# Performance work log

Hardware: AMD Instinct MI355X
Metric: run time of the kernel (lower is better)

The kernel has to match this reference:

```python
import jax, jax.numpy as jnp
import numpy as np

B, S, IN_DIM, D, H, L, C = 8, 1024, 256, 1024, 16, 6, 10
DK = D // H
EPS = 1e-5


def setup_inputs() -> dict:
    key = jax.random.key(0)
    ks = iter(jax.random.split(key, 64))
    n = lambda shape, s=0.02: jax.random.normal(next(ks), shape, dtype=jnp.float32) * s
    inp = {
        'x': jax.random.normal(next(ks), (B, S, IN_DIM), dtype=jnp.float32),
        'emb_w': n((IN_DIM, D)), 'emb_b': jnp.zeros((D,), jnp.float32),
        'Wq': n((L, D, D)), 'bq': jnp.zeros((L, D), jnp.float32),
        'Wk': n((L, D, D)), 'bk': jnp.zeros((L, D), jnp.float32),
        'Wv': n((L, D, D)), 'bv': jnp.zeros((L, D), jnp.float32),
        'Wo': n((L, D, D)), 'bo': jnp.zeros((L, D), jnp.float32),
        'W1': n((L, D, 4 * D)), 'b1': jnp.zeros((L, 4 * D), jnp.float32),
        'W2': n((L, 4 * D, D)), 'b2': jnp.zeros((L, D), jnp.float32),
        'ln1_s': jnp.ones((L, D), jnp.float32), 'ln1_b': jnp.zeros((L, D), jnp.float32),
        'ln2_s': jnp.ones((L, D), jnp.float32), 'ln2_b': jnp.zeros((L, D), jnp.float32),
        'fc_w': n((D, C)), 'fc_b': jnp.zeros((C,), jnp.float32),
    }
    return inp


def _pos_encoding_rows(n_rows):
    # Faithful to the torch module: pe is [max_len,1,D]; pe[:x.size(0)] picks the
    # first `batch` positions and broadcasts over the sequence dim.
    pos = jnp.arange(n_rows, dtype=jnp.float32)[:, None]
    div = jnp.exp(jnp.arange(0, D, 2, dtype=jnp.float32) * (-np.log(10000.0) / D))
    pe = jnp.zeros((n_rows, D), jnp.float32)
    pe = pe.at[:, 0::2].set(jnp.sin(pos * div)).at[:, 1::2].set(jnp.cos(pos * div))
    return pe


def _layer_norm(x, scale, bias):
    mu = jnp.mean(x, axis=-1, keepdims=True)
    var = jnp.mean(jnp.square(x - mu), axis=-1, keepdims=True)
    return (x - mu) * jax.lax.rsqrt(var + EPS) * scale + bias


def reference(x, emb_w, emb_b, Wq, bq, Wk, bk, Wv, bv, Wo, bo,
              W1, b1, W2, b2, ln1_s, ln1_b, ln2_s, ln2_b, fc_w, fc_b):
    h = x @ emb_w + emb_b                              # [B,S,D]
    h = h + _pos_encoding_rows(B)[:, None, :]          # broadcast pe[:B] over seq
    scale = 1.0 / np.sqrt(DK)
    for i in range(L):
        def heads(y, W, b):
            return (y @ W + b).reshape(B, S, H, DK).transpose(0, 2, 1, 3)  # bhsd
        q = heads(h, Wq[i], bq[i])
        k = heads(h, Wk[i], bk[i])
        v = heads(h, Wv[i], bv[i])
        scores = jnp.einsum('bhqd,bhkd->bhqk', q, k) * scale
        p = jax.nn.softmax(scores, axis=-1)
        o = jnp.einsum('bhqk,bhkd->bhqd', p, v)
        o = o.transpose(0, 2, 1, 3).reshape(B, S, D)
        attn_out = o @ Wo[i] + bo[i]
        h = _layer_norm(h + attn_out, ln1_s[i], ln1_b[i])
        ff = jax.nn.relu(h @ W1[i] + b1[i]) @ W2[i] + b2[i]
        h = _layer_norm(h + ff, ln2_s[i], ln2_b[i])
    pooled = jnp.mean(h, axis=1)                       # [B,D]
    return pooled @ fc_w + fc_b                        # [B,C]
```

## Files before the change

kernel.cpp:

```cpp
#include <hip/hip_runtime.h>
#include <stdint.h>

#define B_   8
#define S_   1024
#define IND  256
#define D_   1024
#define H_   16
#define DKH  64
#define L_   6
#define FF   4096
#define NTOK (B_*S_)

typedef __bf16 bf16;
typedef __attribute__((ext_vector_type(4))) float  f32x4;
typedef __attribute__((ext_vector_type(8))) __bf16 bf16x8;
typedef __attribute__((ext_vector_type(4))) __bf16 bf16x4;
typedef __attribute__((ext_vector_type(2))) __bf16 bf16x2;

#define AS1 __attribute__((address_space(1)))
#define AS3 __attribute__((address_space(3)))

__device__ __forceinline__ void gload16(const void* g, void* l) {
  __builtin_amdgcn_global_load_lds((AS1 void*)(const_cast<void*>(g)), (AS3 void*)l, 16, 0, 0);
}

__global__ __launch_bounds__(256)
void k_trans(const float* __restrict__ in, bf16* __restrict__ out,
             int K, int N, long inStride, long outStride) {
  __shared__ float t[32][33];
  const float* inp = in + (long)blockIdx.z * inStride;
  bf16* outp = out + (long)blockIdx.z * outStride;
  const int n0 = blockIdx.x * 32, k0 = blockIdx.y * 32;
  const int tx = threadIdx.x & 31, ty = threadIdx.x >> 5;
  #pragma unroll
  for (int j = 0; j < 32; j += 8)
    t[ty + j][tx] = inp[(long)(k0 + ty + j) * N + n0 + tx];
  __syncthreads();
  #pragma unroll
  for (int j = 0; j < 32; j += 8)
    outp[(long)(n0 + ty + j) * K + k0 + tx] = (bf16)t[tx][ty + j];
}

__global__ __launch_bounds__(256)
void k_f2b(const float* __restrict__ in, bf16* __restrict__ out) {
  const long i = ((long)blockIdx.x * 256 + threadIdx.x) * 4;
  f32x4 v = *(const f32x4*)(in + i);
  bf16x4 o;
  #pragma unroll
  for (int j = 0; j < 4; ++j) o[j] = (bf16)v[j];
  *(bf16x4*)(out + i) = o;
}

__global__ __launch_bounds__(256)
void k_pe(float* __restrict__ pe) {
  const int i = blockIdx.x * 256 + threadIdx.x;
  const int b = i >> 10, d = i & 1023;
  const float k2 = (float)(d & ~1);
  const float dv = __expf(k2 * (-9.210340371976184f / (float)D_));
  const float a = (float)b * dv;
  pe[i] = (d & 1) ? cosf(a) : sinf(a);
}

__global__ __launch_bounds__(256)
void k_packb(const float* __restrict__ bq, const float* __restrict__ bk,
             const float* __restrict__ bv, float* __restrict__ out) {
  const int i = blockIdx.x * 256 + threadIdx.x;
  const int l = i / 3072, j = i % 3072;
  const float* src = (j < 1024) ? bq : ((j < 2048) ? bk : bv);
  out[i] = src[l * 1024 + (j & 1023)];
}

template<int EPI>
__global__ __launch_bounds__(256)
void k_gemm(const bf16* __restrict__ A, const bf16* __restrict__ Bt,
            const float* __restrict__ bias,
            void* __restrict__ out0, void* __restrict__ out1,
            const float* __restrict__ pe,
            int M, int N, int K) {
  __shared__ __align__(16) bf16 sA[128 * 32];
  __shared__ __align__(16) bf16 sB[128 * 32];
  const int tid = threadIdx.x;
  const int lane = tid & 63, wv = tid >> 6;
  const int bx = blockIdx.x, by = blockIdx.y;
  const int wm = wv >> 1, wn = wv & 1;
  const int lg = lane >> 4, lc = lane & 15;
  const long arow0 = (long)by * 128;
  const long brow0 = (long)bx * 128;
  const int c0 = (wv * 2 + 0) * 64 + lane;
  const int c1 = (wv * 2 + 1) * 64 + lane;
  const int r0 = c0 >> 2, s0 = c0 & 3;
  const int r1 = c1 >> 2, s1 = c1 & 3;
  bf16* ldsA0 = sA + (wv * 2 + 0) * 512;
  bf16* ldsA1 = sA + (wv * 2 + 1) * 512;
  bf16* ldsB0 = sB + (wv * 2 + 0) * 512;
  bf16* ldsB1 = sB + (wv * 2 + 1) * 512;
  const bf16* Ab = A + arow0 * K;
  const bf16* Bb = Bt + brow0 * K;
  f32x4 acc[4][4] = {};
  const int kT = K >> 5;
  for (int kt = 0; kt < kT; ++kt) {
    const int k0 = kt << 5;
    gload16(Ab + (long)r0 * K + k0 + s0 * 8, ldsA0);
    gload16(Ab + (long)r1 * K + k0 + s1 * 8, ldsA1);
    gload16(Bb + (long)r0 * K + k0 + s0 * 8, ldsB0);
    gload16(Bb + (long)r1 * K + k0 + s1 * 8, ldsB1);
    __syncthreads();
    bf16x8 af[4], bfr[4];
    #pragma unroll
    for (int mr = 0; mr < 4; ++mr)
      af[mr] = *(const bf16x8*)(sA + (wm * 64 + mr * 16 + lc) * 32 + lg * 8);
    #pragma unroll
    for (int nc = 0; nc < 4; ++nc)
      bfr[nc] = *(const bf16x8*)(sB + (wn * 64 + nc * 16 + lc) * 32 + lg * 8);
    #pragma unroll
    for (int mr = 0; mr < 4; ++mr)
      #pragma unroll
      for (int nc = 0; nc < 4; ++nc)
        acc[mr][nc] = __builtin_amdgcn_mfma_f32_16x16x32_bf16(af[mr], bfr[nc], acc[mr][nc], 0, 0, 0);
    __syncthreads();
  }
  #pragma unroll
  for (int mr = 0; mr < 4; ++mr) {
    const int row0 = by * 128 + wm * 64 + mr * 16 + lg * 4;
    #pragma unroll
    for (int nc = 0; nc < 4; ++nc) {
      const int col = bx * 128 + wn * 64 + nc * 16 + lc;
      const float bvv = bias[col];
      #pragma unroll
      for (int r = 0; r < 4; ++r) {
        float v = acc[mr][nc][r] + bvv;
        const long rr = row0 + r;
        if constexpr (EPI == 0) {
          ((bf16*)out0)[rr * N + col] = (bf16)v;
        } else {
          const long bb = rr >> 10;
          v += pe[bb * D_ + col];
          ((float*)out0)[rr * N + col] = v;
          ((bf16*)out1)[rr * N + col] = (bf16)v;
        }
      }
    }
  }
}

template<int EPI, int SPLIT>
__global__ __launch_bounds__(512, 2)
void k_gemm256(const bf16* __restrict__ A, const bf16* __restrict__ Bt,
               const float* __restrict__ bias,
               void* __restrict__ out0, void* __restrict__ out1,
               bf16* __restrict__ pout0, bf16* __restrict__ pout1,
               int M, int N, int K) {
  __shared__ __align__(16) bf16 lds[65536];
  const int tid = threadIdx.x;
  const int lane = tid & 63, wv = tid >> 6;
  const int wm = wv >> 2, wn = wv & 3;
  const int lg = lane >> 4, lc = lane & 15;
  const int gx = gridDim.x;
  const int nwg = gx * gridDim.y;
  int bid = blockIdx.x + blockIdx.y * gx;
  const int cpx = nwg >> 3;
  bid = (bid & 7) * cpx + (bid >> 3);
  const int bxs = bid % gx, bys = bid / gx;
  const int tileRow = bys * 256, tileCol = bxs * 256;
  const int kPart = SPLIT ? (K >> 1) : K;
  const long kOff = SPLIT ? (long)blockIdx.z * kPart : 0;
  const bf16* Abase = A + (long)tileRow * K + kOff;
  const bf16* Bbase = Bt + (long)tileCol * K + kOff;
  const long laneOff = (long)lc * K + lg * 8;
  f32x4 acc[8][4] = {};
  const int NT = kPart >> 6;
  const int NI = NT >> 1;

  auto stA = [&](int t, int h, int bb) {
    const int rg = h * 16 + wv * 2;
    const int mb = rg >> 1;
    const bf16* s = Abase + (long)(mb * 16) * K + t * 64 + laneOff;
    bf16* d = lds + bb * 32768 + rg * 512;
    gload16(s, d);
    gload16(s + 32, d + 512);
  };
  auto stB = [&](int t, int h, int bb) {
    const int rg = h * 16 + wv * 2;
    const int mb = rg >> 1;
    const bf16* s = Bbase + (long)(mb * 16) * K + t * 64 + laneOff;
    bf16* d = lds + bb * 32768 + 16384 + rg * 512;
    gload16(s, d);
    gload16(s + 32, d + 512);
  };

  bf16x8 aF[8];
  bf16x8 bF0[4], bF1[4];

#define LDA(BB, MH) do { _Pragma("unroll") for (int m = 0; m < 4; ++m) \
    _Pragma("unroll") for (int kk = 0; kk < 2; ++kk) \
      aF[m*2+kk] = *(const bf16x8*)(lds + (BB)*32768 + ((wm*8 + (MH)*4 + m)*2 + kk)*512 + lane*8); \
  } while(0)
#define LDB(BB, NH, DST) do { _Pragma("unroll") for (int n = 0; n < 2; ++n) \
    _Pragma("unroll") for (int kk = 0; kk < 2; ++kk) \
      DST[n*2+kk] = *(const bf16x8*)(lds + (BB)*32768 + 16384 + ((wn*4 + (NH)*2 + n)*2 + kk)*512 + lane*8); \
  } while(0)
#define MMA(MH, NH, BSRC) do { \
    __builtin_amdgcn_s_setprio(1); \
    _Pragma("unroll") for (int m = 0; m < 4; ++m) \
      _Pragma("unroll") for (int n = 0; n < 2; ++n) { \
        acc[(MH)*4+m][(NH)*2+n] = __builtin_amdgcn_mfma_f32_16x16x32_bf16(aF[m*2+0], BSRC[n*2+0], acc[(MH)*4+m][(NH)*2+n], 0, 0, 0); \
        acc[(MH)*4+m][(NH)*2+n] = __builtin_amdgcn_mfma_f32_16x16x32_bf16(aF[m*2+1], BSRC[n*2+1], acc[(MH)*4+m][(NH)*2+n], 0, 0, 0); \
      } \
    __builtin_amdgcn_s_setprio(0); \
  } while(0)
#define VM8 asm volatile("s_waitcnt vmcnt(8)" ::: "memory")
#define VM0 asm volatile("s_waitcnt vmcnt(0)" ::: "memory")
#define BAR __builtin_amdgcn_s_barrier()

  stA(0, 0, 0); stB(0, 0, 0); stA(0, 1, 0); stB(0, 1, 0);
  stA(1, 0, 1); stB(1, 0, 1); stA(1, 1, 1); stB(1, 1, 1);

  for (int i = 0; i < NI - 1; ++i) {
    const int t2 = 2 * i + 2, t3 = 2 * i + 3;
    VM8; BAR; LDA(0, 0); LDB(0, 0, bF0);   MMA(0, 0, bF0);
         BAR; LDB(0, 1, bF1); stA(t2, 0, 0);              MMA(0, 1, bF1);
         BAR; LDA(0, 1);      stB(t2, 0, 0);              MMA(1, 0, bF0);
         BAR; stA(t2, 1, 0);  stB(t2, 1, 0);              MMA(1, 1, bF1);
    VM8; BAR; LDA(1, 0); LDB(1, 0, bF0);   MMA(0, 0, bF0);
         BAR; LDB(1, 1, bF1); stA(t3, 0, 1);              MMA(0, 1, bF1);
         BAR; LDA(1, 1);      stB(t3, 0, 1);              MMA(1, 0, bF0);
         BAR; stA(t3, 1, 1);  stB(t3, 1, 1);              MMA(1, 1, bF1);
  }
  {
    VM8; BAR; LDA(0, 0); LDB(0, 0, bF0); MMA(0, 0, bF0);
         BAR; LDB(0, 1, bF1);            MMA(0, 1, bF1);
         BAR; LDA(0, 1);                 MMA(1, 0, bF0);
         BAR;                            MMA(1, 1, bF1);
    VM0; BAR; LDA(1, 0); LDB(1, 0, bF0); MMA(0, 0, bF0);
         BAR; LDB(1, 1, bF1);            MMA(0, 1, bF1);
         BAR; LDA(1, 1);                 MMA(1, 0, bF0);
         BAR;                            MMA(1, 1, bF1);
  }
#undef LDA
#undef LDB
#undef MMA
#undef VM8
#undef VM0
#undef BAR

  #pragma unroll
  for (int mr = 0; mr < 8; ++mr) {
    const int row0 = tileRow + wm * 128 + mr * 16 + lg * 4;
    #pragma unroll
    for (int nr = 0; nr < 4; ++nr) {
      const int col = tileCol + wn * 64 + nr * 16 + lc;
      if constexpr (SPLIT) {
        bf16* po = blockIdx.z ? pout1 : pout0;
        #pragma unroll
        for (int r = 0; r < 4; ++r)
          po[(long)(row0 + r) * N + col] = (bf16)acc[mr][nr][r];
      } else if constexpr (EPI == 2) {
        const float bvv = bias[col];
        const int which = col >> 10;
        const int hh = (col & 1023) >> 6;
        const int dk = col & 63;
        const long bb = row0 >> 10;
        const int sr = row0 & 1023;
        if (which == 2) {
          bf16x4 pk;
          #pragma unroll
          for (int r = 0; r < 4; ++r) pk[r] = (bf16)(acc[mr][nr][r] + bvv);
          *(bf16x4*)((bf16*)out1 + ((bb * H_ + hh) * (long)DKH + dk) * S_ + sr) = pk;
        } else {
          #pragma unroll
          for (int r = 0; r < 4; ++r) {
            float v = acc[mr][nr][r] + bvv;
            if (which == 0) v *= 0.125f;
            ((bf16*)out0)[(long)which * NTOK * D_ + ((bb * H_ + hh) * (long)S_ + sr + r) * DKH + dk] = (bf16)v;
          }
        }
      } else {
        const float bvv = bias[col];
        #pragma unroll
        for (int r = 0; r < 4; ++r) {
          float v = acc[mr][nr][r] + bvv;
          const long rr = row0 + r;
          if constexpr (EPI == 1) v = fmaxf(v, 0.f);
          ((bf16*)out0)[rr * N + col] = (bf16)v;
        }
      }
    }
  }
}

__global__ __launch_bounds__(256)
void k_flash(const bf16* __restrict__ qg, const bf16* __restrict__ kgl,
             const bf16* __restrict__ vtg, bf16* __restrict__ og) {
  __shared__ __align__(16) bf16 sK[64 * 64];
  __shared__ __align__(16) bf16 sV[64 * 64];
  __shared__ __align__(16) bf16 sP[4 * 16 * 64];
  const int tid = threadIdx.x, lane = tid & 63, wv = tid >> 6;
  const int lg = lane >> 4, lc = lane & 15;
  int bid = blockIdx.x + blockIdx.y * 16;
  bid = (bid & 7) * 256 + (bid >> 3);
  const int qt = bid & 15, bh = bid >> 4;
  const long base = (long)bh * S_ * DKH;
  const bf16* qb = qg + base;
  const bf16* kb = kgl + base;
  const bf16* vb = vtg + base;
  const int qrow = qt * 64 + wv * 16 + lc;
  const bf16x8 qf0 = *(const bf16x8*)(qb + (long)qrow * DKH + lg * 8);
  const bf16x8 qf1 = *(const bf16x8*)(qb + (long)qrow * DKH + 32 + lg * 8);
  float mrun = -3e38f, lrun = 0.f;
  f32x4 oacc[4] = {};
  bf16* sPw = sP + wv * (16 * 64);
  const int swzP = (lc & 7) << 4;
  const int c0 = wv * 128 + lane, c1 = c0 + 64;
  const int r0 = c0 >> 3, sl0 = (c0 & 7) ^ (r0 & 7);
  const int r1 = c1 >> 3, sl1 = (c1 & 7) ^ (r1 & 7);
  bf16* dst0 = sK + c0 * 8 - lane * 8;
  bf16* dst1 = sK + c1 * 8 - lane * 8;
  bf16* dstV0 = sV + c0 * 8 - lane * 8;
  bf16* dstV1 = sV + c1 * 8 - lane * 8;
  for (int kt = 0; kt < S_ / 64; ++kt) {
    const int gk = kt * 64;
    gload16(kb + (long)(gk + r0) * DKH + sl0 * 8, dst0);
    gload16(kb + (long)(gk + r1) * DKH + sl1 * 8, dst1);
    gload16(vb + (long)r0 * S_ + gk + sl0 * 8, dstV0);
    gload16(vb + (long)r1 * S_ + gk + sl1 * 8, dstV1);
    __syncthreads();
    f32x4 sacc[4] = {};
    #pragma unroll
    for (int nc = 0; nc < 4; ++nc) {
      const int kr = nc * 16 + lc;
      bf16x8 k0 = *(const bf16x8*)((char*)sK + kr * 128 + (((0 + lg) ^ (kr & 7)) << 4));
      bf16x8 k1 = *(const bf16x8*)((char*)sK + kr * 128 + (((4 + lg) ^ (kr & 7)) << 4));
      sacc[nc] = __builtin_amdgcn_mfma_f32_16x16x32_bf16(k0, qf0, sacc[nc], 0, 0, 0);
      sacc[nc] = __builtin_amdgcn_mfma_f32_16x16x32_bf16(k1, qf1, sacc[nc], 0, 0, 0);
    }
    float pm = sacc[0][0];
    #pragma unroll
    for (int nc = 0; nc < 4; ++nc)
      #pragma unroll
      for (int r = 0; r < 4; ++r) pm = fmaxf(pm, sacc[nc][r]);
    pm = fmaxf(pm, __shfl_xor(pm, 16));
    pm = fmaxf(pm, __shfl_xor(pm, 32));
    const float mnew = fmaxf(mrun, pm);
    const float fac = __expf(mrun - mnew);
    float ps = 0.f;
    #pragma unroll
    for (int nc = 0; nc < 4; ++nc)
      #pragma unroll
      for (int r = 0; r < 4; ++r) {
        const float p = __expf(sacc[nc][r] - mnew);
        sacc[nc][r] = p;
        ps += p;
      }
    ps += __shfl_xor(ps, 16);
    ps += __shfl_xor(ps, 32);
    lrun = lrun * fac + ps;
    mrun = mnew;
    #pragma unroll
    for (int nc = 0; nc < 4; ++nc)
      #pragma unroll
      for (int rp = 0; rp < 2; ++rp) {
        bf16x2 t;
        t[0] = (bf16)sacc[nc][rp * 2 + 0];
        t[1] = (bf16)sacc[nc][rp * 2 + 1];
        *(bf16x2*)((char*)sPw + lc * 128 + ((nc * 32 + lg * 8 + rp * 4) ^ swzP)) = t;
      }
    asm volatile("s_waitcnt lgkmcnt(0)" ::: "memory");
    __builtin_amdgcn_sched_barrier(0);
    float fr[4];
    #pragma unroll
    for (int r = 0; r < 4; ++r) fr[r] = __shfl(fac, lg * 4 + r);
    #pragma unroll
    for (int nc = 0; nc < 4; ++nc)
      #pragma unroll
      for (int r = 0; r < 4; ++r) oacc[nc][r] *= fr[r];
    #pragma unroll
    for (int m = 0; m < 2; ++m) {
      const bf16x8 pf = *(const bf16x8*)((char*)sPw + lc * 128 + ((m * 64 + lg * 16) ^ swzP));
      #pragma unroll
      for (int nc = 0; nc < 4; ++nc) {
        const int vr = nc * 16 + lc;
        bf16x8 vf = *(const bf16x8*)((char*)sV + vr * 128 + (((m * 4 + lg) ^ (vr & 7)) << 4));
        oacc[nc] = __builtin_amdgcn_mfma_f32_16x16x32_bf16(pf, vf, oacc[nc], 0, 0, 0);
      }
    }
    __syncthreads();
  }
  const int b = bh >> 4, h = bh & 15;
  const float linv = 1.f / lrun;
  #pragma unroll
  for (int r = 0; r < 4; ++r) {
    const float inv = __shfl(linv, lg * 4 + r);
    const int s = qt * 64 + wv * 16 + lg * 4 + r;
    const long obase = (((long)b * S_ + s) * H_ + h) * DKH;
    #pragma unroll
    for (int nc = 0; nc < 4; ++nc)
      og[obase + nc * 16 + lc] = (bf16)(oacc[nc][r] * inv);
  }
}

template<int TWO>
__global__ __launch_bounds__(256)
void k_addln(const float* __restrict__ hin, const bf16* __restrict__ dlt,
             const bf16* __restrict__ p0, const bf16* __restrict__ p1,
             const float* __restrict__ gb,
             const float* __restrict__ sc, const float* __restrict__ bi,
             float* __restrict__ hout, bf16* __restrict__ hbout) {
  const int row = blockIdx.x, t = threadIdx.x;
  const long off = (long)row * D_ + t * 4;
  f32x4 hv = *(const f32x4*)(hin + off);
  f32x4 x;
  if constexpr (TWO) {
    bf16x4 a = *(const bf16x4*)(p0 + off);
    bf16x4 b = *(const bf16x4*)(p1 + off);
    f32x4 g = *(const f32x4*)(gb + t * 4);
    #pragma unroll
    for (int j = 0; j < 4; ++j) x[j] = hv[j] + (float)a[j] + (float)b[j] + g[j];
  } else {
    bf16x4 dv = *(const bf16x4*)(dlt + off);
    #pragma unroll
    for (int j = 0; j < 4; ++j) x[j] = hv[j] + (float)dv[j];
  }
  float s = 0.f, ss = 0.f;
  #pragma unroll
  for (int j = 0; j < 4; ++j) { s += x[j]; ss += x[j] * x[j]; }
  #pragma unroll
  for (int m = 1; m < 64; m <<= 1) { s += __shfl_xor(s, m); ss += __shfl_xor(ss, m); }
  __shared__ float red[8];
  const int w = t >> 6, ln = t & 63;
  if (ln == 0) { red[w] = s; red[4 + w] = ss; }
  __syncthreads();
  s = red[0] + red[1] + red[2] + red[3];
  ss = red[4] + red[5] + red[6] + red[7];
  const float mu = s * (1.f / D_);
  const float rstd = rsqrtf(ss * (1.f / D_) - mu * mu + 1e-5f);
  f32x4 scv = *(const f32x4*)(sc + t * 4);
  f32x4 biv = *(const f32x4*)(bi + t * 4);
  f32x4 y; bf16x4 yb;
  #pragma unroll
  for (int j = 0; j < 4; ++j) { y[j] = (x[j] - mu) * rstd * scv[j] + biv[j]; yb[j] = (bf16)y[j]; }
  *(f32x4*)(hout + off) = y;
  *(bf16x4*)(hbout + off) = yb;
}

__global__ __launch_bounds__(256)
void k_pool1(const float* __restrict__ h, float* __restrict__ part) {
  const int i = blockIdx.x * 256 + threadIdx.x;
  const int b = i >> 10, d = i & 1023;
  const int s0 = blockIdx.y * 128;
  float s = 0.f;
  for (int t = 0; t < 128; ++t) s += h[((long)b * S_ + s0 + t) * D_ + d];
  part[(long)blockIdx.y * NTOK + i] = s;
}

__global__ __launch_bounds__(256)
void k_pool2(const float* __restrict__ part, float* __restrict__ pooled) {
  const int i = blockIdx.x * 256 + threadIdx.x;
  float s = 0.f;
  #pragma unroll
  for (int j = 0; j < 8; ++j) s += part[(long)j * NTOK + i];
  pooled[i] = s * (1.f / S_);
}

__global__ __launch_bounds__(64)
void k_fc(const float* __restrict__ pooled, const float* __restrict__ fw,
          const float* __restrict__ fb, float* __restrict__ out) {
  const int b = blockIdx.x / 10, c = blockIdx.x % 10;
  const int lane = threadIdx.x;
  float s = 0.f;
  for (int d = lane; d < D_; d += 64) s += pooled[b * D_ + d] * fw[d * 10 + c];
  #pragma unroll
  for (int m = 1; m < 64; m <<= 1) s += __shfl_xor(s, m);
  if (lane == 0) out[b * 10 + c] = s + fb[c];
}

extern "C" void kernel_launch(void* const* d_in, const int* in_sizes, int n_in,
                              void* d_out, int out_size, void* d_ws, size_t ws_size,
                              hipStream_t stream) {
  const float* x     = (const float*)d_in[0];
  const float* emb_w = (const float*)d_in[1];
  const float* emb_b = (const float*)d_in[2];
  const float* Wq    = (const float*)d_in[3];
  const float* bq    = (const float*)d_in[4];
  const float* Wk    = (const float*)d_in[5];
  const float* bk    = (const float*)d_in[6];
  const float* Wv    = (const float*)d_in[7];
  const float* bv    = (const float*)d_in[8];
  const float* Wo    = (const float*)d_in[9];
  const float* bo    = (const float*)d_in[10];
  const float* W1    = (const float*)d_in[11];
  const float* b1    = (const float*)d_in[12];
  const float* W2    = (const float*)d_in[13];
  const float* b2    = (const float*)d_in[14];
  const float* ln1s  = (const float*)d_in[15];
  const float* ln1b  = (const float*)d_in[16];
  const float* ln2s  = (const float*)d_in[17];
  const float* ln2b  = (const float*)d_in[18];
  const float* fcw   = (const float*)d_in[19];
  const float* fcb   = (const float*)d_in[20];

  char* w = (char*)d_ws;
  size_t off = 0;
  auto alloc = [&](size_t bytes) -> char* {
    char* p = w + off;
    off += (bytes + 255) & ~(size_t)255;
    return p;
  };
  bf16*  x_bf  = (bf16*) alloc((size_t)NTOK * IND * 2);
  bf16*  embT  = (bf16*) alloc((size_t)D_ * IND * 2);
  bf16*  qkvT  = (bf16*) alloc((size_t)L_ * 3 * D_ * D_ * 2);
  bf16*  woT   = (bf16*) alloc((size_t)L_ * D_ * D_ * 2);
  bf16*  w1T   = (bf16*) alloc((size_t)L_ * FF * D_ * 2);
  bf16*  w2T   = (bf16*) alloc((size_t)L_ * D_ * FF * 2);
  float* qkvB  = (float*)alloc((size_t)L_ * 3 * D_ * 4);
  float* pe    = (float*)alloc((size_t)B_ * D_ * 4);
  float* h_f   = (float*)alloc((size_t)NTOK * D_ * 4);
  bf16*  h_b   = (bf16*) alloc((size_t)NTOK * D_ * 2);
  bf16*  delta = (bf16*) alloc((size_t)NTOK * D_ * 2);
  float* pooled= (float*)alloc((size_t)B_ * D_ * 4);
  float* part  = (float*)alloc((size_t)8 * NTOK * 4);
  bf16*  scratch = (bf16*)alloc((size_t)NTOK * FF * 2);
  bf16* qb  = scratch;
  bf16* kb  = scratch + (size_t)NTOK * D_;
  bf16* vTb = scratch + (size_t)2 * NTOK * D_;
  bf16* ob  = scratch + (size_t)3 * NTOK * D_;
  bf16* ffn1 = scratch;
  bf16* p0 = (bf16*)alloc((size_t)NTOK * D_ * 2);
  bf16* p1 = (bf16*)alloc((size_t)NTOK * D_ * 2);
  const bool canSplit = (off <= ws_size);
  (void)in_sizes; (void)n_in; (void)out_size;

  k_f2b<<<dim3(NTOK * IND / 1024), dim3(256), 0, stream>>>(x, x_bf);
  k_trans<<<dim3(D_ / 32, IND / 32, 1), dim3(256), 0, stream>>>(emb_w, embT, IND, D_, 0, 0);
  k_trans<<<dim3(32, 32, L_), dim3(256), 0, stream>>>(Wq, qkvT,               D_, D_, (long)D_ * D_, (long)3 * D_ * D_);
  k_trans<<<dim3(32, 32, L_), dim3(256), 0, stream>>>(Wk, qkvT + D_ * D_,     D_, D_, (long)D_ * D_, (long)3 * D_ * D_);
  k_trans<<<dim3(32, 32, L_), dim3(256), 0, stream>>>(Wv, qkvT + 2 * D_ * D_, D_, D_, (long)D_ * D_, (long)3 * D_ * D_);
  k_trans<<<dim3(32, 32, L_), dim3(256), 0, stream>>>(Wo, woT, D_, D_, (long)D_ * D_, (long)D_ * D_);
  k_trans<<<dim3(FF / 32, 32, L_), dim3(256), 0, stream>>>(W1, w1T, D_, FF, (long)D_ * FF, (long)FF * D_);
  k_trans<<<dim3(32, FF / 32, L_), dim3(256), 0, stream>>>(W2, w2T, FF, D_, (long)FF * D_, (long)D_ * FF);
  k_pe<<<dim3(B_ * D_ / 256), dim3(256), 0, stream>>>(pe);
  k_packb<<<dim3(L_ * 3 * D_ / 256), dim3(256), 0, stream>>>(bq, bk, bv, qkvB);

  k_gemm<3><<<dim3(D_ / 128, NTOK / 128), dim3(256), 0, stream>>>(
      x_bf, embT, emb_b, h_f, h_b, pe, NTOK, D_, IND);

  for (int l = 0; l < L_; ++l) {
    k_gemm256<2, 0><<<dim3(3 * D_ / 256, NTOK / 256), dim3(512), 0, stream>>>(
        h_b, qkvT + (size_t)l * 3 * D_ * D_, qkvB + l * 3 * D_,
        qb, vTb, nullptr, nullptr, NTOK, 3 * D_, D_);
    k_flash<<<dim3(S_ / 64, B_ * H_), dim3(256), 0, stream>>>(qb, kb, vTb, ob);
    if (canSplit) {
      k_gemm256<0, 1><<<dim3(D_ / 256, NTOK / 256, 2), dim3(512), 0, stream>>>(
          ob, woT + (size_t)l * D_ * D_, nullptr,
          nullptr, nullptr, p0, p1, NTOK, D_, D_);
      k_addln<1><<<dim3(NTOK), dim3(256), 0, stream>>>(
          h_f, nullptr, p0, p1, bo + l * D_, ln1s + l * D_, ln1b + l * D_, h_f, h_b);
    } else {
      k_gemm256<0, 0><<<dim3(D_ / 256, NTOK / 256), dim3(512), 0, stream>>>(
          ob, woT + (size_t)l * D_ * D_, bo + l * D_,
          delta, nullptr, nullptr, nullptr, NTOK, D_, D_);
      k_addln<0><<<dim3(NTOK), dim3(256), 0, stream>>>(
          h_f, delta, nullptr, nullptr, nullptr, ln1s + l * D_, ln1b + l * D_, h_f, h_b);
    }
    k_gemm256<1, 0><<<dim3(FF / 256, NTOK / 256), dim3(512), 0, stream>>>(
        h_b, w1T + (size_t)l * FF * D_, b1 + l * FF,
        ffn1, nullptr, nullptr, nullptr, NTOK, FF, D_);
    if (canSplit) {
      k_gemm256<0, 1><<<dim3(D_ / 256, NTOK / 256, 2), dim3(512), 0, stream>>>(
          ffn1, w2T + (size_t)l * D_ * FF, nullptr,
          nullptr, nullptr, p0, p1, NTOK, D_, FF);
      k_addln<1><<<dim3(NTOK), dim3(256), 0, stream>>>(
          h_f, nullptr, p0, p1, b2 + l * D_, ln2s + l * D_, ln2b + l * D_, h_f, h_b);
    } else {
      k_gemm256<0, 0><<<dim3(D_ / 256, NTOK / 256), dim3(512), 0, stream>>>(
          ffn1, w2T + (size_t)l * D_ * FF, b2 + l * D_,
          delta, nullptr, nullptr, nullptr, NTOK, D_, FF);
      k_addln<0><<<dim3(NTOK), dim3(256), 0, stream>>>(
          h_f, delta, nullptr, nullptr, nullptr, ln2s + l * D_, ln2b + l * D_, h_f, h_b);
    }
  }

  k_pool1<<<dim3(NTOK / 256, 8), dim3(256), 0, stream>>>(h_f, part);
  k_pool2<<<dim3(NTOK / 256), dim3(256), 0, stream>>>(part, pooled);
  k_fc<<<dim3(B_ * 10), dim3(64), 0, stream>>>(pooled, fcw, fcb, (float*)d_out);
}
```

Before: 2.287 ms.

## Drop fp32 residual stream and add 128x256-tile QKV GEMM kernel

The fp32 copy of the hidden state is removed, so the residual add, layer norm and pooling now read and write only the bf16 activation buffer. This cuts memory traffic in the add+layernorm kernels and the embedding epilogue. It also adds a dedicated QKV projection GEMM with 128x256 tiles and a head-split epilogue, which doubles the number of workgroups for better CU occupancy. The price is lower residual precision, since bf16 rounding now accumulates across layers.

```diff
diff --git a/kernel.cpp b/kernel.cpp
--- a/kernel.cpp
+++ b/kernel.cpp
@@ -135,7 +135,6 @@
         } else {
           const long bb = rr >> 10;
           v += pe[bb * D_ + col];
-          ((float*)out0)[rr * N + col] = v;
           ((bf16*)out1)[rr * N + col] = (bf16)v;
         }
       }
@@ -254,26 +253,6 @@
         #pragma unroll
         for (int r = 0; r < 4; ++r)
           po[(long)(row0 + r) * N + col] = (bf16)acc[mr][nr][r];
-      } else if constexpr (EPI == 2) {
-        const float bvv = bias[col];
-        const int which = col >> 10;
-        const int hh = (col & 1023) >> 6;
-        const int dk = col & 63;
-        const long bb = row0 >> 10;
-        const int sr = row0 & 1023;
-        if (which == 2) {
-          bf16x4 pk;
-          #pragma unroll
-          for (int r = 0; r < 4; ++r) pk[r] = (bf16)(acc[mr][nr][r] + bvv);
-          *(bf16x4*)((bf16*)out1 + ((bb * H_ + hh) * (long)DKH + dk) * S_ + sr) = pk;
-        } else {
-          #pragma unroll
-          for (int r = 0; r < 4; ++r) {
-            float v = acc[mr][nr][r] + bvv;
-            if (which == 0) v *= 0.125f;
-            ((bf16*)out0)[(long)which * NTOK * D_ + ((bb * H_ + hh) * (long)S_ + sr + r) * DKH + dk] = (bf16)v;
-          }
-        }
       } else {
         const float bvv = bias[col];
         #pragma unroll
@@ -282,6 +261,127 @@
           const long rr = row0 + r;
           if constexpr (EPI == 1) v = fmaxf(v, 0.f);
           ((bf16*)out0)[rr * N + col] = (bf16)v;
+        }
+      }
+    }
+  }
+}
+
+__global__ __launch_bounds__(512, 2)
+void k_gemmQ(const bf16* __restrict__ A, const bf16* __restrict__ Bt,
+             const float* __restrict__ bias,
+             bf16* __restrict__ out0, bf16* __restrict__ out1,
+             int M, int N, int K) {
+  __shared__ __align__(16) bf16 lds[49152];
+  const int tid = threadIdx.x;
+  const int lane = tid & 63, wv = tid >> 6;
+  const int wm = wv >> 2, wn = wv & 3;
+  const int lg = lane >> 4, lc = lane & 15;
+  const int gx = gridDim.x;
+  const int nwg = gx * gridDim.y;
+  int bid = blockIdx.x + blockIdx.y * gx;
+  const int cpx = nwg >> 3;
+  bid = (bid & 7) * cpx + (bid >> 3);
+  const int bxs = bid % gx, bys = bid / gx;
+  const int tileRow = bys * 128, tileCol = bxs * 256;
+  const bf16* Abase = A + (long)tileRow * K;
+  const bf16* Bbase = Bt + (long)tileCol * K;
+  const long laneOff = (long)lc * K + lg * 8;
+  f32x4 acc[4][4] = {};
+  const int NT = K >> 6;
+  const int NI = NT >> 1;
+
+  auto stA = [&](int t, int bb) {
+    const bf16* s = Abase + (long)(wv * 16) * K + t * 64 + laneOff;
+    bf16* d = lds + bb * 24576 + (wv * 2) * 512;
+    gload16(s, d);
+    gload16(s + 32, d + 512);
+  };
+  auto stB = [&](int t, int h, int bb) {
+    const bf16* s = Bbase + (long)((wv * 2 + h) * 16) * K + t * 64 + laneOff;
+    bf16* d = lds + bb * 24576 + 8192 + (wv * 4 + h * 2) * 512;
+    gload16(s, d);
+    gload16(s + 32, d + 512);
+  };
+
+  bf16x8 aF[4];
+  bf16x8 bF0[4], bF1[4];
+
+#define LDA(BB, MH) do { _Pragma("unroll") for (int m = 0; m < 2; ++m) \
+    _Pragma("unroll") for (int kk = 0; kk < 2; ++kk) \
+      aF[m*2+kk] = *(const bf16x8*)(lds + (BB)*24576 + ((wm*4 + (MH)*2 + m)*2 + kk)*512 + lane*8); \
+  } while(0)
+#define LDB(BB, NH, DST) do { _Pragma("unroll") for (int n = 0; n < 2; ++n) \
+    _Pragma("unroll") for (int kk = 0; kk < 2; ++kk) \
+      DST[n*2+kk] = *(const bf16x8*)(lds + (BB)*24576 + 8192 + ((wn*4 + (NH)*2 + n)*2 + kk)*512 + lane*8); \
+  } while(0)
+#define MMA(MH, NH, BSRC) do { \
+    __builtin_amdgcn_s_setprio(1); \
+    _Pragma("unroll") for (int m = 0; m < 2; ++m) \
+      _Pragma("unroll") for (int n = 0; n < 2; ++n) { \
+        acc[(MH)*2+m][(NH)*2+n] = __builtin_amdgcn_mfma_f32_16x16x32_bf16(aF[m*2+0], BSRC[n*2+0], acc[(MH)*2+m][(NH)*2+n], 0, 0, 0); \
+        acc[(MH)*2+m][(NH)*2+n] = __builtin_amdgcn_mfma_f32_16x16x32_bf16(aF[m*2+1], BSRC[n*2+1], acc[(MH)*2+m][(NH)*2+n], 0, 0, 0); \
+      } \
+    __builtin_amdgcn_s_setprio(0); \
+  } while(0)
+#define VM6 asm volatile("s_waitcnt vmcnt(6)" ::: "memory")
+#define VM0 asm volatile("s_waitcnt vmcnt(0)" ::: "memory")
+#define BAR __builtin_amdgcn_s_barrier()
+
+  stA(0, 0); stB(0, 0, 0); stB(0, 1, 0);
+  stA(1, 1); stB(1, 0, 1); stB(1, 1, 1);
+
+  for (int i = 0; i < NI - 1; ++i) {
+    const int t2 = 2 * i + 2, t3 = 2 * i + 3;
+    VM6; BAR; LDA(0, 0); LDB(0, 0, bF0);   MMA(0, 0, bF0);
+         BAR; LDB(0, 1, bF1); stA(t2, 0);              MMA(0, 1, bF1);
+         BAR; LDA(0, 1);      stB(t2, 0, 0);           MMA(1, 0, bF0);
+         BAR;                 stB(t2, 1, 0);           MMA(1, 1, bF1);
+    VM6; BAR; LDA(1, 0); LDB(1, 0, bF0);   MMA(0, 0, bF0);
+         BAR; LDB(1, 1, bF1); stA(t3, 1);              MMA(0, 1, bF1);
+         BAR; LDA(1, 1);      stB(t3, 0, 1);           MMA(1, 0, bF0);
+         BAR;                 stB(t3, 1, 1);           MMA(1, 1, bF1);
+  }
+  {
+    VM6; BAR; LDA(0, 0); LDB(0, 0, bF0); MMA(0, 0, bF0);
+         BAR; LDB(0, 1, bF1);            MMA(0, 1, bF1);
+         BAR; LDA(0, 1);                 MMA(1, 0, bF0);
+         BAR;                            MMA(1, 1, bF1);
+    VM0; BAR; LDA(1, 0); LDB(1, 0, bF0); MMA(0, 0, bF0);
+         BAR; LDB(1, 1, bF1);            MMA(0, 1, bF1);
+         BAR; LDA(1, 1);                 MMA(1, 0, bF0);
+         BAR;                            MMA(1, 1, bF1);
+  }
+#undef LDA
+#undef LDB
+#undef MMA
+#undef VM6
+#undef VM0
+#undef BAR
+
+  #pragma unroll
+  for (int mr = 0; mr < 4; ++mr) {
+    const int row0 = tileRow + wm * 64 + mr * 16 + lg * 4;
+    #pragma unroll
+    for (int nr = 0; nr < 4; ++nr) {
+      const int col = tileCol + wn * 64 + nr * 16 + lc;
+      const float bvv = bias[col];
+      const int which = col >> 10;
+      const int hh = (col & 1023) >> 6;
+      const int dk = col & 63;
+      const long bb = row0 >> 10;
+      const int sr = row0 & 1023;
+      if (which == 2) {
+        bf16x4 pk;
+        #pragma unroll
+        for (int r = 0; r < 4; ++r) pk[r] = (bf16)(acc[mr][nr][r] + bvv);
+        *(bf16x4*)(out1 + ((bb * H_ + hh) * (long)DKH + dk) * S_ + sr) = pk;
+      } else {
+        #pragma unroll
+        for (int r = 0; r < 4; ++r) {
+          float v = acc[mr][nr][r] + bvv;
+          if (which == 0) v *= 0.125f;
+          out0[(long)which * NTOK * D_ + ((bb * H_ + hh) * (long)S_ + sr + r) * DKH + dk] = (bf16)v;
         }
       }
     }
@@ -400,25 +500,25 @@
 
 template<int TWO>
 __global__ __launch_bounds__(256)
-void k_addln(const float* __restrict__ hin, const bf16* __restrict__ dlt,
+void k_addln(const bf16* __restrict__ hin, const bf16* __restrict__ dlt,
              const bf16* __restrict__ p0, const bf16* __restrict__ p1,
              const float* __restrict__ gb,
              const float* __restrict__ sc, const float* __restrict__ bi,
-             float* __restrict__ hout, bf16* __restrict__ hbout) {
+             bf16* __restrict__ hbout) {
   const int row = blockIdx.x, t = threadIdx.x;
   const long off = (long)row * D_ + t * 4;
-  f32x4 hv = *(const f32x4*)(hin + off);
+  bf16x4 hv = *(const bf16x4*)(hin + off);
   f32x4 x;
   if constexpr (TWO) {
     bf16x4 a = *(const bf16x4*)(p0 + off);
     bf16x4 b = *(const bf16x4*)(p1 + off);
     f32x4 g = *(const f32x4*)(gb + t * 4);
     #pragma unroll
-    for (int j = 0; j < 4; ++j) x[j] = hv[j] + (float)a[j] + (float)b[j] + g[j];
+    for (int j = 0; j < 4; ++j) x[j] = (float)hv[j] + (float)a[j] + (float)b[j] + g[j];
   } else {
     bf16x4 dv = *(const bf16x4*)(dlt + off);
     #pragma unroll
-    for (int j = 0; j < 4; ++j) x[j] = hv[j] + (float)dv[j];
+    for (int j = 0; j < 4; ++j) x[j] = (float)hv[j] + (float)dv[j];
   }
   float s = 0.f, ss = 0.f;
   #pragma unroll
@@ -435,20 +535,19 @@
   const float rstd = rsqrtf(ss * (1.f / D_) - mu * mu + 1e-5f);
   f32x4 scv = *(const f32x4*)(sc + t * 4);
   f32x4 biv = *(const f32x4*)(bi + t * 4);
-  f32x4 y; bf16x4 yb;
-  #pragma unroll
-  for (int j = 0; j < 4; ++j) { y[j] = (x[j] - mu) * rstd * scv[j] + biv[j]; yb[j] = (bf16)y[j]; }
-  *(f32x4*)(hout + off) = y;
+  bf16x4 yb;
+  #pragma unroll
+  for (int j = 0; j < 4; ++j) yb[j] = (bf16)((x[j] - mu) * rstd * scv[j] + biv[j]);
   *(bf16x4*)(hbout + off) = yb;
 }
 
 __global__ __launch_bounds__(256)
-void k_pool1(const float* __restrict__ h, float* __restrict__ part) {
+void k_pool1(const bf16* __restrict__ h, float* __restrict__ part) {
   const int i = blockIdx.x * 256 + threadIdx.x;
   const int b = i >> 10, d = i & 1023;
   const int s0 = blockIdx.y * 128;
   float s = 0.f;
-  for (int t = 0; t < 128; ++t) s += h[((long)b * S_ + s0 + t) * D_ + d];
+  for (int t = 0; t < 128; ++t) s += (float)h[((long)b * S_ + s0 + t) * D_ + d];
   part[(long)blockIdx.y * NTOK + i] = s;
 }
 
@@ -513,7 +612,6 @@
   bf16*  w2T   = (bf16*) alloc((size_t)L_ * D_ * FF * 2);
   float* qkvB  = (float*)alloc((size_t)L_ * 3 * D_ * 4);
   float* pe    = (float*)alloc((size_t)B_ * D_ * 4);
-  float* h_f   = (float*)alloc((size_t)NTOK * D_ * 4);
   bf16*  h_b   = (bf16*) alloc((size_t)NTOK * D_ * 2);
   bf16*  delta = (bf16*) alloc((size_t)NTOK * D_ * 2);
   float* pooled= (float*)alloc((size_t)B_ * D_ * 4);
@@ -541,25 +639,25 @@
   k_packb<<<dim3(L_ * 3 * D_ / 256), dim3(256), 0, stream>>>(bq, bk, bv, qkvB);
 
   k_gemm<3><<<dim3(D_ / 128, NTOK / 128), dim3(256), 0, stream>>>(
-      x_bf, embT, emb_b, h_f, h_b, pe, NTOK, D_, IND);
+      x_bf, embT, emb_b, nullptr, h_b, pe, NTOK, D_, IND);
 
   for (int l = 0; l < L_; ++l) {
-    k_gemm256<2, 0><<<dim3(3 * D_ / 256, NTOK / 256), dim3(512), 0, stream>>>(
+    k_gemmQ<<<dim3(3 * D_ / 256, NTOK / 128), dim3(512), 0, stream>>>(
         h_b, qkvT + (size_t)l * 3 * D_ * D_, qkvB + l * 3 * D_,
-        qb, vTb, nullptr, nullptr, NTOK, 3 * D_, D_);
+        qb, vTb, NTOK, 3 * D_, D_);
     k_flash<<<dim3(S_ / 64, B_ * H_), dim3(256), 0, stream>>>(qb, kb, vTb, ob);
     if (canSplit) {
       k_gemm256<0, 1><<<dim3(D_ / 256, NTOK / 256, 2), dim3(512), 0, stream>>>(
           ob, woT + (size_t)l * D_ * D_, nullptr,
           nullptr, nullptr, p0, p1, NTOK, D_, D_);
       k_addln<1><<<dim3(NTOK), dim3(256), 0, stream>>>(
-          h_f, nullptr, p0, p1, bo + l * D_, ln1s + l * D_, ln1b + l * D_, h_f, h_b);
+          h_b, nullptr, p0, p1, bo + l * D_, ln1s + l * D_, ln1b + l * D_, h_b);
     } else {
       k_gemm256<0, 0><<<dim3(D_ / 256, NTOK / 256), dim3(512), 0, stream>>>(
           ob, woT + (size_t)l * D_ * D_, bo + l * D_,
           delta, nullptr, nullptr, nullptr, NTOK, D_, D_);
       k_addln<0><<<dim3(NTOK), dim3(256), 0, stream>>>(
-          h_f, delta, nullptr, nullptr, nullptr, ln1s + l * D_, ln1b + l * D_, h_f, h_b);
+          h_b, delta, nullptr, nullptr, nullptr, ln1s + l * D_, ln1b + l * D_, h_b);
     }
     k_gemm256<1, 0><<<dim3(FF / 256, NTOK / 256), dim3(512), 0, stream>>>(
         h_b, w1T + (size_t)l * FF * D_, b1 + l * FF,
@@ -569,17 +667,17 @@
           ffn1, w2T + (size_t)l * D_ * FF, nullptr,
           nullptr, nullptr, p0, p1, NTOK, D_, FF);
       k_addln<1><<<dim3(NTOK), dim3(256), 0, stream>>>(
-          h_f, nullptr, p0, p1, b2 + l * D_, ln2s + l * D_, ln2b + l * D_, h_f, h_b);
+          h_b, nullptr, p0, p1, b2 + l * D_, ln2s + l * D_, ln2b + l * D_, h_b);
     } else {
       k_gemm256<0, 0><<<dim3(D_ / 256, NTOK / 256), dim3(512), 0, stream>>>(
           ffn1, w2T + (size_t)l * D_ * FF, b2 + l * D_,
           delta, nullptr, nullptr, nullptr, NTOK, D_, FF);
       k_addln<0><<<dim3(NTOK), dim3(256), 0, stream>>>(
-          h_f, delta, nullptr, nullptr, nullptr, ln2s + l * D_, ln2b + l * D_, h_f, h_b);
+          h_b, delta, nullptr, nullptr, nullptr, ln2s + l * D_, ln2b + l * D_, h_b);
     }
   }
 
-  k_pool1<<<dim3(NTOK / 256, 8), dim3(256), 0, stream>>>(h_f, part);
+  k_pool1<<<dim3(NTOK / 256, 8), dim3(256), 0, stream>>>(h_b, part);
   k_pool2<<<dim3(NTOK / 256), dim3(256), 0, stream>>>(part, pooled);
   k_fc<<<dim3(B_ * 10), dim3(64), 0, stream>>>(pooled, fcw, fcb, (float*)d_out);
 }
```

Result: faster. 2.211 ms (-3.3%).

## Keep residual stream in bf16 only and vectorize weight transpose

Applied to the files above, without the earlier changes.

Drops the fp32 copy of the hidden state. Residual adds, layer norms and pooling now read and write only the bf16 buffer, which removes an fp32 read and write of the full activation tensor in every add+layernorm and in the embedding epilogue. The weight transpose kernel also moves to 64x64 tiles with float4 loads and bf16x4 stores to cut per-element memory traffic. The cost is precision: the residual stream is rounded to bf16 after every layer, which can add accumulated error over six layers.

```diff
diff --git a/kernel.cpp b/kernel.cpp
--- a/kernel.cpp
+++ b/kernel.cpp
@@ -27,18 +27,27 @@
 __global__ __launch_bounds__(256)
 void k_trans(const float* __restrict__ in, bf16* __restrict__ out,
              int K, int N, long inStride, long outStride) {
-  __shared__ float t[32][33];
+  __shared__ float t[64][65];
   const float* inp = in + (long)blockIdx.z * inStride;
   bf16* outp = out + (long)blockIdx.z * outStride;
-  const int n0 = blockIdx.x * 32, k0 = blockIdx.y * 32;
-  const int tx = threadIdx.x & 31, ty = threadIdx.x >> 5;
-  #pragma unroll
-  for (int j = 0; j < 32; j += 8)
-    t[ty + j][tx] = inp[(long)(k0 + ty + j) * N + n0 + tx];
+  const int n0 = blockIdx.x * 64, k0 = blockIdx.y * 64;
+  const int r = threadIdx.x >> 4;
+  const int c4 = (threadIdx.x & 15) * 4;
+  #pragma unroll
+  for (int j = 0; j < 64; j += 16) {
+    f32x4 v = *(const f32x4*)(inp + (long)(k0 + r + j) * N + n0 + c4);
+    #pragma unroll
+    for (int i = 0; i < 4; ++i) t[r + j][c4 + i] = v[i];
+  }
   __syncthreads();
   #pragma unroll
-  for (int j = 0; j < 32; j += 8)
-    outp[(long)(n0 + ty + j) * K + k0 + tx] = (bf16)t[tx][ty + j];
+  for (int j = 0; j < 64; j += 16) {
+    const int n = r + j;
+    bf16x4 o;
+    #pragma unroll
+    for (int i = 0; i < 4; ++i) o[i] = (bf16)t[c4 + i][n];
+    *(bf16x4*)(outp + (long)(n0 + n) * K + k0 + c4) = o;
+  }
 }
 
 __global__ __launch_bounds__(256)
@@ -135,7 +144,6 @@
         } else {
           const long bb = rr >> 10;
           v += pe[bb * D_ + col];
-          ((float*)out0)[rr * N + col] = v;
           ((bf16*)out1)[rr * N + col] = (bf16)v;
         }
       }
@@ -400,25 +408,25 @@
 
 template<int TWO>
 __global__ __launch_bounds__(256)
-void k_addln(const float* __restrict__ hin, const bf16* __restrict__ dlt,
+void k_addln(const bf16* __restrict__ hin, const bf16* __restrict__ dlt,
              const bf16* __restrict__ p0, const bf16* __restrict__ p1,
              const float* __restrict__ gb,
              const float* __restrict__ sc, const float* __restrict__ bi,
-             float* __restrict__ hout, bf16* __restrict__ hbout) {
+             bf16* __restrict__ hbout) {
   const int row = blockIdx.x, t = threadIdx.x;
   const long off = (long)row * D_ + t * 4;
-  f32x4 hv = *(const f32x4*)(hin + off);
+  bf16x4 hv = *(const bf16x4*)(hin + off);
   f32x4 x;
   if constexpr (TWO) {
     bf16x4 a = *(const bf16x4*)(p0 + off);
     bf16x4 b = *(const bf16x4*)(p1 + off);
     f32x4 g = *(const f32x4*)(gb + t * 4);
     #pragma unroll
-    for (int j = 0; j < 4; ++j) x[j] = hv[j] + (float)a[j] + (float)b[j] + g[j];
+    for (int j = 0; j < 4; ++j) x[j] = (float)hv[j] + (float)a[j] + (float)b[j] + g[j];
   } else {
     bf16x4 dv = *(const bf16x4*)(dlt + off);
     #pragma unroll
-    for (int j = 0; j < 4; ++j) x[j] = hv[j] + (float)dv[j];
+    for (int j = 0; j < 4; ++j) x[j] = (float)hv[j] + (float)dv[j];
   }
   float s = 0.f, ss = 0.f;
   #pragma unroll
@@ -435,20 +443,19 @@
   const float rstd = rsqrtf(ss * (1.f / D_) - mu * mu + 1e-5f);
   f32x4 scv = *(const f32x4*)(sc + t * 4);
   f32x4 biv = *(const f32x4*)(bi + t * 4);
-  f32x4 y; bf16x4 yb;
-  #pragma unroll
-  for (int j = 0; j < 4; ++j) { y[j] = (x[j] - mu) * rstd * scv[j] + biv[j]; yb[j] = (bf16)y[j]; }
-  *(f32x4*)(hout + off) = y;
+  bf16x4 yb;
+  #pragma unroll
+  for (int j = 0; j < 4; ++j) yb[j] = (bf16)((x[j] - mu) * rstd * scv[j] + biv[j]);
   *(bf16x4*)(hbout + off) = yb;
 }
 
 __global__ __launch_bounds__(256)
-void k_pool1(const float* __restrict__ h, float* __restrict__ part) {
+void k_pool1(const bf16* __restrict__ h, float* __restrict__ part) {
   const int i = blockIdx.x * 256 + threadIdx.x;
   const int b = i >> 10, d = i & 1023;
   const int s0 = blockIdx.y * 128;
   float s = 0.f;
-  for (int t = 0; t < 128; ++t) s += h[((long)b * S_ + s0 + t) * D_ + d];
+  for (int t = 0; t < 128; ++t) s += (float)h[((long)b * S_ + s0 + t) * D_ + d];
   part[(long)blockIdx.y * NTOK + i] = s;
 }
 
@@ -513,7 +520,6 @@
   bf16*  w2T   = (bf16*) alloc((size_t)L_ * D_ * FF * 2);
   float* qkvB  = (float*)alloc((size_t)L_ * 3 * D_ * 4);
   float* pe    = (float*)alloc((size_t)B_ * D_ * 4);
-  float* h_f   = (float*)alloc((size_t)NTOK * D_ * 4);
   bf16*  h_b   = (bf16*) alloc((size_t)NTOK * D_ * 2);
   bf16*  delta = (bf16*) alloc((size_t)NTOK * D_ * 2);
   float* pooled= (float*)alloc((size_t)B_ * D_ * 4);
@@ -530,18 +536,18 @@
   (void)in_sizes; (void)n_in; (void)out_size;
 
   k_f2b<<<dim3(NTOK * IND / 1024), dim3(256), 0, stream>>>(x, x_bf);
-  k_trans<<<dim3(D_ / 32, IND / 32, 1), dim3(256), 0, stream>>>(emb_w, embT, IND, D_, 0, 0);
-  k_trans<<<dim3(32, 32, L_), dim3(256), 0, stream>>>(Wq, qkvT,               D_, D_, (long)D_ * D_, (long)3 * D_ * D_);
-  k_trans<<<dim3(32, 32, L_), dim3(256), 0, stream>>>(Wk, qkvT + D_ * D_,     D_, D_, (long)D_ * D_, (long)3 * D_ * D_);
-  k_trans<<<dim3(32, 32, L_), dim3(256), 0, stream>>>(Wv, qkvT + 2 * D_ * D_, D_, D_, (long)D_ * D_, (long)3 * D_ * D_);
-  k_trans<<<dim3(32, 32, L_), dim3(256), 0, stream>>>(Wo, woT, D_, D_, (long)D_ * D_, (long)D_ * D_);
-  k_trans<<<dim3(FF / 32, 32, L_), dim3(256), 0, stream>>>(W1, w1T, D_, FF, (long)D_ * FF, (long)FF * D_);
-  k_trans<<<dim3(32, FF / 32, L_), dim3(256), 0, stream>>>(W2, w2T, FF, D_, (long)FF * D_, (long)D_ * FF);
+  k_trans<<<dim3(D_ / 64, IND / 64, 1), dim3(256), 0, stream>>>(emb_w, embT, IND, D_, 0, 0);
+  k_trans<<<dim3(D_ / 64, D_ / 64, L_), dim3(256), 0, stream>>>(Wq, qkvT,               D_, D_, (long)D_ * D_, (long)3 * D_ * D_);
+  k_trans<<<dim3(D_ / 64, D_ / 64, L_), dim3(256), 0, stream>>>(Wk, qkvT + D_ * D_,     D_, D_, (long)D_ * D_, (long)3 * D_ * D_);
+  k_trans<<<dim3(D_ / 64, D_ / 64, L_), dim3(256), 0, stream>>>(Wv, qkvT + 2 * D_ * D_, D_, D_, (long)D_ * D_, (long)3 * D_ * D_);
+  k_trans<<<dim3(D_ / 64, D_ / 64, L_), dim3(256), 0, stream>>>(Wo, woT, D_, D_, (long)D_ * D_, (long)D_ * D_);
+  k_trans<<<dim3(FF / 64, D_ / 64, L_), dim3(256), 0, stream>>>(W1, w1T, D_, FF, (long)D_ * FF, (long)FF * D_);
+  k_trans<<<dim3(D_ / 64, FF / 64, L_), dim3(256), 0, stream>>>(W2, w2T, FF, D_, (long)FF * D_, (long)D_ * FF);
   k_pe<<<dim3(B_ * D_ / 256), dim3(256), 0, stream>>>(pe);
   k_packb<<<dim3(L_ * 3 * D_ / 256), dim3(256), 0, stream>>>(bq, bk, bv, qkvB);
 
   k_gemm<3><<<dim3(D_ / 128, NTOK / 128), dim3(256), 0, stream>>>(
-      x_bf, embT, emb_b, h_f, h_b, pe, NTOK, D_, IND);
+      x_bf, embT, emb_b, nullptr, h_b, pe, NTOK, D_, IND);
 
   for (int l = 0; l < L_; ++l) {
     k_gemm256<2, 0><<<dim3(3 * D_ / 256, NTOK / 256), dim3(512), 0, stream>>>(
@@ -553,13 +559,13 @@
           ob, woT + (size_t)l * D_ * D_, nullptr,
           nullptr, nullptr, p0, p1, NTOK, D_, D_);
       k_addln<1><<<dim3(NTOK), dim3(256), 0, stream>>>(
-          h_f, nullptr, p0, p1, bo + l * D_, ln1s + l * D_, ln1b + l * D_, h_f, h_b);
+          h_b, nullptr, p0, p1, bo + l * D_, ln1s + l * D_, ln1b + l * D_, h_b);
     } else {
       k_gemm256<0, 0><<<dim3(D_ / 256, NTOK / 256), dim3(512), 0, stream>>>(
           ob, woT + (size_t)l * D_ * D_, bo + l * D_,
           delta, nullptr, nullptr, nullptr, NTOK, D_, D_);
       k_addln<0><<<dim3(NTOK), dim3(256), 0, stream>>>(
-          h_f, delta, nullptr, nullptr, nullptr, ln1s + l * D_, ln1b + l * D_, h_f, h_b);
+          h_b, delta, nullptr, nullptr, nullptr, ln1s + l * D_, ln1b + l * D_, h_b);
     }
     k_gemm256<1, 0><<<dim3(FF / 256, NTOK / 256), dim3(512), 0, stream>>>(
         h_b, w1T + (size_t)l * FF * D_, b1 + l * FF,
@@ -569,17 +575,17 @@
           ffn1, w2T + (size_t)l * D_ * FF, nullptr,
           nullptr, nullptr, p0, p1, NTOK, D_, FF);
       k_addln<1><<<dim3(NTOK), dim3(256), 0, stream>>>(
-          h_f, nullptr, p0, p1, b2 + l * D_, ln2s + l * D_, ln2b + l * D_, h_f, h_b);
+          h_b, nullptr, p0, p1, b2 + l * D_, ln2s + l * D_, ln2b + l * D_, h_b);
     } else {
       k_gemm256<0, 0><<<dim3(D_ / 256, NTOK / 256), dim3(512), 0, stream>>>(
           ffn1, w2T + (size_t)l * D_ * FF, b2 + l * D_,
           delta, nullptr, nullptr, nullptr, NTOK, D_, FF);
       k_addln<0><<<dim3(NTOK), dim3(256), 0, stream>>>(
-          h_f, delta, nullptr, nullptr, nullptr, ln2s + l * D_, ln2b + l * D_, h_f, h_b);
+          h_b, delta, nullptr, nullptr, nullptr, ln2s + l * D_, ln2b + l * D_, h_b);
     }
   }
 
-  k_pool1<<<dim3(NTOK / 256, 8), dim3(256), 0, stream>>>(h_f, part);
+  k_pool1<<<dim3(NTOK / 256, 8), dim3(256), 0, stream>>>(h_b, part);
   k_pool2<<<dim3(NTOK / 256), dim3(256), 0, stream>>>(part, pooled);
   k_fc<<<dim3(B_ * 10), dim3(64), 0, stream>>>(pooled, fcw, fcb, (float*)d_out);
 }
```

Measured after the change: 2.180 ms, median of 3. 4.7% less time.
